# Kernel tuning notes

Measured on AMD Instinct MI355X. Metric: run time of the kernel, lower is better.

## Reference

```python
import jax, jax.numpy as jnp
import numpy as np

TAU = 0.05


def _normalize(x):
    return x / jnp.linalg.norm(x, axis=-1, keepdims=True)


def setup_inputs() -> dict:
    key = jax.random.key(0)
    ks = jax.random.split(key, 7)
    D, S, Q, N, P = 256, 64, 4096, 16384, 1024
    return {
        "article_emb": jax.random.normal(ks[0], (D,), dtype=jnp.float32),
        "section_embs": jax.random.normal(ks[1], (S, D), dtype=jnp.float32),
        "question_embs": jax.random.normal(ks[2], (Q, D), dtype=jnp.float32),
        "sentence_embs": jax.random.normal(ks[3], (N, D), dtype=jnp.float32),
        "paragraph_idx_for_question": jax.random.randint(ks[4], (Q,), 0, P, dtype=jnp.int32),
        "section_idx_for_question": jax.random.randint(ks[5], (Q,), 0, S, dtype=jnp.int32),
        "sent_paragraph_idx": jax.random.randint(ks[6], (N,), 0, P, dtype=jnp.int32),
        "num_paragraphs": P,
    }


def reference(article_emb, section_embs, question_embs, sentence_embs,
              paragraph_idx_for_question, section_idx_for_question,
              sent_paragraph_idx, num_paragraphs):
    tau = TAU
    dt = question_embs.dtype
    # normalize (article is normalized in the original but unused in the loss; AT_loss == 0)
    _ = _normalize(article_emb)
    sec = _normalize(section_embs)   # [S, D]
    que = _normalize(question_embs)  # [Q, D]
    sen = _normalize(sentence_embs)  # [N, D]
    Q, N = que.shape[0], sen.shape[0]
    S = sec.shape[0]

    # ---------- QS debiased InfoNCE ----------
    sim_qs = jnp.matmul(que, sen.T) / tau              # [Q, N]
    exp_qs = jnp.exp(sim_qs)                           # [Q, N]
    pos = paragraph_idx_for_question[:, None] == sent_paragraph_idx[None, :]  # [Q, N]
    M = pos.sum(axis=1)                                # positives per question
    Nn = N - M                                         # negatives per question
    sum_pos = jnp.where(pos, exp_qs, 0.0).sum(axis=1)
    sum_neg = exp_qs.sum(axis=1) - sum_pos
    eta_plus = 1.0 / max(int(num_paragraphs), 1)
    eta_minus = 1.0 - eta_plus
    min_val = jnp.exp(jnp.asarray(-1.0 / tau, dtype=dt))
    M_f = jnp.maximum(M, 1).astype(dt)
    Nn_f = jnp.maximum(Nn, 1).astype(dt)
    g = jnp.maximum((sum_neg / Nn_f - eta_plus * sum_pos / M_f) / eta_minus, min_val)  # [Q]
    valid = (M > 0) & (Nn > 0)                         # [Q]
    # -log(numer / (numer + N_neg * g)) = -(sim - log(denom))
    denom_qs = exp_qs + (Nn.astype(dt) * g)[:, None]
    log_ratio_qs = sim_qs - jnp.log(denom_qs)
    mask_qs = pos & valid[:, None]
    total_qs = jnp.where(valid, M, 0).sum()
    qs_loss = -jnp.where(mask_qs, log_ratio_qs, 0.0).sum()
    qs_loss = jnp.where(total_qs > 0, qs_loss / total_qs.astype(dt), jnp.asarray(0.0, dt))

    # ---------- SQ InfoNCE ----------
    sim_sq = jnp.matmul(sec, que.T) / tau              # [S, Q]
    exp_sq = jnp.exp(sim_sq)
    posq = section_idx_for_question[None, :] == jnp.arange(S)[:, None]  # [S, Q]
    Mq = posq.sum(axis=1)
    Nnq = Q - Mq
    sum_neg_q = exp_sq.sum(axis=1) - jnp.where(posq, exp_sq, 0.0).sum(axis=1)  # [S]
    log_ratio_sq = sim_sq - jnp.log(exp_sq + sum_neg_q[:, None])
    validq = (Mq > 0) & (Nnq > 0)
    mask_sq = posq & validq[:, None]
    total_sq = jnp.where(validq, Mq, 0).sum()
    sq_loss = -jnp.where(mask_sq, log_ratio_sq, 0.0).sum()
    sq_loss = jnp.where(total_sq > 0, sq_loss / total_sq.astype(dt), jnp.asarray(0.0, dt))

    return qs_loss + sq_loss
```

## Files before the change

### kernel.cpp

```cpp
#include <hip/hip_runtime.h>
#include <hip/hip_bf16.h>
#include <math.h>

#define D 256
#define INV_TAU 20.0f
#define CAP 64
#define PBUF 128
#define ACC2S (INV_TAU / 256.0f)
#define K2F (ACC2S * 1.4426950408889634f)

typedef __attribute__((ext_vector_type(4))) float f32x4;

#define GLOAD16(gp, lp) \
    __builtin_amdgcn_global_load_lds((const __attribute__((address_space(1))) void*)(gp), \
                                     (__attribute__((address_space(3))) void*)(lp), 16, 0, 0)

__global__ void norm_all(const float* __restrict__ que, const float* __restrict__ sen,
                         const float* __restrict__ sec,
                         unsigned char* __restrict__ queb, unsigned char* __restrict__ senb,
                         unsigned char* __restrict__ secb, int Q, int N, int S) {
    int r = blockIdx.x * 4 + (threadIdx.x >> 6);
    int lane = threadIdx.x & 63;
    if (r >= Q + N + S) return;
    const float* src; unsigned char* dst; int row;
    if (r < Q) { src = que; dst = queb; row = r; }
    else if (r < Q + N) { src = sen; dst = senb; row = r - Q; }
    else { src = sec; dst = secb; row = r - Q - N; }
    const float4* p = (const float4*)(src + (size_t)row * D);
    float4 v = p[lane];
    float ss = v.x * v.x + v.y * v.y + v.z * v.z + v.w * v.w;
    #pragma unroll
    for (int m = 1; m < 64; m <<= 1) ss += __shfl_xor(ss, m);
    float s = rsqrtf(ss) * 16.0f;
    int pk = __builtin_amdgcn_cvt_pk_fp8_f32(v.x * s, v.y * s, 0, false);
    pk = __builtin_amdgcn_cvt_pk_fp8_f32(v.z * s, v.w * s, pk, true);
    int wg = (lane >> 1) & 7;
    int pos = (wg < 4) ? (2 * wg) : (2 * (wg - 4) + 1);
    int byte = ((lane >> 4) << 6) + (pos << 3) + ((lane & 1) << 2);
    *(int*)(dst + (size_t)row * D + byte) = pk;
}

__global__ __launch_bounds__(256, 4)
void qs_sq(const unsigned char* __restrict__ queb, const unsigned char* __restrict__ senb,
           const unsigned char* __restrict__ secb,
           const int* __restrict__ pidq, const int* __restrict__ pidn,
           const int* __restrict__ sidx, int Q,
           float* __restrict__ partial, int* __restrict__ cnt, float* __restrict__ pos_s,
           float* __restrict__ sq_all, float* __restrict__ sq_pos, int* __restrict__ sq_m,
           float* __restrict__ simq) {
    __shared__ unsigned char As[128 * 64];
    __shared__ unsigned char Bs[128 * 64];
    __shared__ int pqs[128];
    __shared__ int pns[128];
    __shared__ float sums[2][128];
    __shared__ int lcnt;
    __shared__ int lq[PBUF];
    __shared__ float lsv[PBUF];

    const int tid = threadIdx.x;
    const int lane = tid & 63;
    const int cl = lane & 15;
    const int g = lane >> 4;
    const int wid = tid >> 6;
    const int bid = blockIdx.x;
    const int nsq = Q >> 7;

    if (bid < nsq) {
        const int q0 = bid * 128;
        const int qw = q0 + wid * 32;
        f32x4 acc[4][2];
        #pragma unroll
        for (int si = 0; si < 4; ++si)
            #pragma unroll
            for (int qi = 0; qi < 2; ++qi)
                acc[si][qi] = (f32x4){0.f, 0.f, 0.f, 0.f};
        const unsigned char* abase = secb + (size_t)cl * D + g * 16;
        const unsigned char* bbase = queb + (size_t)(qw + cl) * D + g * 16;
        #pragma unroll
        for (int b = 0; b < 4; ++b) {
            const int k0 = b * 64;
            long2 af[4], bq[2];
            #pragma unroll
            for (int si = 0; si < 4; ++si)
                af[si] = *(const long2*)(abase + (size_t)si * 16 * D + k0);
            #pragma unroll
            for (int qi = 0; qi < 2; ++qi)
                bq[qi] = *(const long2*)(bbase + (size_t)qi * 16 * D + k0);
            #pragma unroll
            for (int si = 0; si < 4; ++si)
                #pragma unroll
                for (int qi = 0; qi < 2; ++qi) {
                    acc[si][qi] = __builtin_amdgcn_mfma_f32_16x16x32_fp8_fp8(af[si].x, bq[qi].x, acc[si][qi], 0, 0, 0);
                    acc[si][qi] = __builtin_amdgcn_mfma_f32_16x16x32_fp8_fp8(af[si].y, bq[qi].y, acc[si][qi], 0, 0, 0);
                }
        }
        int sidxv[2];
        sidxv[0] = sidx[qw + cl];
        sidxv[1] = sidx[qw + 16 + cl];
        #pragma unroll
        for (int si = 0; si < 4; ++si) {
            float pa[4] = {0.f, 0.f, 0.f, 0.f};
            #pragma unroll
            for (int qi = 0; qi < 2; ++qi) {
                #pragma unroll
                for (int j = 0; j < 4; ++j) {
                    int srow = si * 16 + g * 4 + j;
                    float sv = acc[si][qi][j] * ACC2S;
                    float e = __expf(sv);
                    pa[j] += e;
                    if (sidxv[qi] == srow) {
                        int q = qw + qi * 16 + cl;
                        simq[q] = sv;
                        atomicAdd(&sq_pos[srow], e);
                        atomicAdd(&sq_m[srow], 1);
                    }
                }
            }
            #pragma unroll
            for (int j = 0; j < 4; ++j) {
                float a = pa[j];
                #pragma unroll
                for (int msk = 1; msk < 16; msk <<= 1) a += __shfl_xor(a, msk);
                if (cl == 0) atomicAdd(&sq_all[si * 16 + g * 4 + j], a);
            }
        }
        return;
    }

    const int qbid = bid - nsq;
    const int qt = qbid & 31;
    const int nt = qbid >> 5;
    const int wr = wid >> 1, wc = wid & 1;
    const int q0 = qt * 128;
    const int n0 = nt * 128;

    if (tid < 128) pqs[tid] = pidq[q0 + tid];
    else           pns[tid - 128] = pidn[n0 + tid - 128];
    if (tid == 0) lcnt = 0;

    const int r0s = tid >> 2;
    const int c0s = tid & 3;
    const unsigned char* qa0 = queb + (size_t)(q0 + r0s) * D + ((c0s ^ ((r0s >> 1) & 3)) << 4);
    const unsigned char* qa1 = queb + (size_t)(q0 + 64 + r0s) * D + ((c0s ^ (((r0s + 64) >> 1) & 3)) << 4);
    const unsigned char* sb0 = senb + (size_t)(n0 + r0s) * D + ((c0s ^ ((r0s >> 1) & 3)) << 4);
    const unsigned char* sb1 = senb + (size_t)(n0 + 64 + r0s) * D + ((c0s ^ (((r0s + 64) >> 1) & 3)) << 4);
    const int ld0 = wid * 1024;
    const int ld1 = 4096 + wid * 1024;

#define STAGE(k0) do { \
    GLOAD16(qa0 + (k0), &As[ld0]); \
    GLOAD16(qa1 + (k0), &As[ld1]); \
    GLOAD16(sb0 + (k0), &Bs[ld0]); \
    GLOAD16(sb1 + (k0), &Bs[ld1]); \
} while (0)

    f32x4 acc[4][4];
    #pragma unroll
    for (int m = 0; m < 4; ++m)
        #pragma unroll
        for (int n = 0; n < 4; ++n)
            acc[m][n] = (f32x4){0.f, 0.f, 0.f, 0.f};

    const int fsw = (g ^ ((cl >> 1) & 3)) << 4;
    int offA[4], offB[4];
    #pragma unroll
    for (int m = 0; m < 4; ++m) offA[m] = (wr * 64 + m * 16 + cl) * 64 + fsw;
    #pragma unroll
    for (int n = 0; n < 4; ++n) offB[n] = (wc * 64 + n * 16 + cl) * 64 + fsw;

    STAGE(0);
    #pragma unroll
    for (int ks = 0; ks < 4; ++ks) {
        __syncthreads();
        long2 af[4], bg[4];
        #pragma unroll
        for (int m = 0; m < 4; ++m) af[m] = *(const long2*)&As[offA[m]];
        #pragma unroll
        for (int n = 0; n < 4; ++n) bg[n] = *(const long2*)&Bs[offB[n]];
        #pragma unroll
        for (int m = 0; m < 4; ++m)
            #pragma unroll
            for (int n = 0; n < 4; ++n)
                acc[m][n] = __builtin_amdgcn_mfma_f32_16x16x32_fp8_fp8(af[m].x, bg[n].x, acc[m][n], 0, 0, 0);
        #pragma unroll
        for (int m = 0; m < 4; ++m)
            #pragma unroll
            for (int n = 0; n < 4; ++n)
                acc[m][n] = __builtin_amdgcn_mfma_f32_16x16x32_fp8_fp8(af[m].y, bg[n].y, acc[m][n], 0, 0, 0);
        if (ks < 3) {
            __syncthreads();
            STAGE((ks + 1) * 64);
        }
    }
#undef STAGE

    #pragma unroll
    for (int m = 0; m < 4; ++m) {
        float se[4] = {0.f, 0.f, 0.f, 0.f};
        int pqr[4];
        #pragma unroll
        for (int j = 0; j < 4; ++j) pqr[j] = pqs[wr * 64 + m * 16 + g * 4 + j];
        #pragma unroll
        for (int n = 0; n < 4; ++n) {
            const int pcol = pns[wc * 64 + n * 16 + cl];
            #pragma unroll
            for (int j = 0; j < 4; ++j) {
                float e = __builtin_amdgcn_exp2f(acc[m][n][j] * K2F);
                se[j] += e;
                if (pqr[j] == pcol) {
                    int li = atomicAdd(&lcnt, 1);
                    if (li < PBUF) {
                        lq[li] = q0 + wr * 64 + m * 16 + g * 4 + j;
                        lsv[li] = acc[m][n][j] * ACC2S;
                    }
                }
            }
        }
        #pragma unroll
        for (int j = 0; j < 4; ++j) {
            float a = se[j];
            #pragma unroll
            for (int msk = 1; msk < 16; msk <<= 1) a += __shfl_xor(a, msk);
            if (cl == 0) sums[wc][wr * 64 + m * 16 + g * 4 + j] = a;
        }
    }
    __syncthreads();
    if (tid < 128)
        partial[(size_t)nt * Q + q0 + tid] = sums[0][tid] + sums[1][tid];
    int nc = lcnt < PBUF ? lcnt : PBUF;
    for (int i = tid; i < nc; i += 256) {
        int q = lq[i];
        int idx = atomicAdd(&cnt[q], 1);
        if (idx < CAP) pos_s[(size_t)q * CAP + idx] = lsv[i];
    }
}

__global__ __launch_bounds__(256)
void finish(const float* __restrict__ partial, int NSLICE,
            const int* __restrict__ cnt, const float* __restrict__ pos_s,
            const int* __restrict__ sidx, const float* __restrict__ simq,
            const float* __restrict__ sq_all, const float* __restrict__ sq_pos,
            const int* __restrict__ sq_m,
            const int* __restrict__ npp, int Qn, int Ntot,
            float* __restrict__ bpart) {
    __shared__ float fred[4][4];
    const int tid = threadIdx.x, lane = tid & 63, wid = tid >> 6;
    const int q = blockIdx.x * 4 + wid;

    float Sa = 0.f;
    for (int nb = lane; nb < NSLICE; nb += 64) Sa += partial[(size_t)nb * Qn + q];
    #pragma unroll
    for (int m = 1; m < 64; m <<= 1) Sa += __shfl_xor(Sa, m);

    int M = cnt[q];
    int mc = M < CAP ? M : CAP;
    float s = 0.f, e = 0.f;
    if (lane < mc) { s = pos_s[(size_t)q * CAP + lane]; e = __expf(s); }
    float Sp = e;
    #pragma unroll
    for (int m = 1; m < 64; m <<= 1) Sp += __shfl_xor(Sp, m);

    int Nn = Ntot - M;
    int P = npp[0];
    float eta_p = 1.0f / (float)(P > 1 ? P : 1);
    float eta_m = 1.0f - eta_p;
    float Mf = (float)(M > 1 ? M : 1);
    float Nnf = (float)(Nn > 1 ? Nn : 1);
    float gg = fmaxf(((Sa - Sp) / Nnf - eta_p * Sp / Mf) / eta_m, __expf(-INV_TAU));
    float c = (float)Nn * gg;

    float contrib = (lane < mc) ? (s - __logf(e + c)) : 0.f;
    #pragma unroll
    for (int m = 1; m < 64; m <<= 1) contrib += __shfl_xor(contrib, m);

    if (lane == 0) {
        float qs_num = 0.f, qs_cnt = 0.f, sq_num = 0.f, sq_cnt = 0.f;
        if (M > 0 && Nn > 0) { qs_num = contrib; qs_cnt = (float)M; }
        int sct = sidx[q];
        int Mq = sq_m[sct];
        if (Mq > 0 && (Qn - Mq) > 0) {
            float sv = simq[q];
            float sumneg = sq_all[sct] - sq_pos[sct];
            sq_num = sv - __logf(__expf(sv) + sumneg);
            sq_cnt = 1.f;
        }
        fred[wid][0] = qs_num; fred[wid][1] = qs_cnt;
        fred[wid][2] = sq_num; fred[wid][3] = sq_cnt;
    }
    __syncthreads();
    if (tid < 4) {
        float v = fred[0][tid] + fred[1][tid] + fred[2][tid] + fred[3][tid];
        bpart[(size_t)blockIdx.x * 4 + tid] = v;
    }
}

__global__ void combine2(const float* __restrict__ bpart, int nblk, float* __restrict__ out) {
    __shared__ float r2[4][4];
    const int tid = threadIdx.x, lane = tid & 63, wid = tid >> 6;
    float v[4] = {0.f, 0.f, 0.f, 0.f};
    for (int i = tid; i < nblk; i += 256) {
        #pragma unroll
        for (int c2 = 0; c2 < 4; ++c2) v[c2] += bpart[(size_t)i * 4 + c2];
    }
    #pragma unroll
    for (int m = 1; m < 64; m <<= 1)
        #pragma unroll
        for (int c2 = 0; c2 < 4; ++c2) v[c2] += __shfl_xor(v[c2], m);
    if (lane == 0) {
        #pragma unroll
        for (int c2 = 0; c2 < 4; ++c2) r2[wid][c2] = v[c2];
    }
    __syncthreads();
    if (tid == 0) {
        float qs_num = r2[0][0] + r2[1][0] + r2[2][0] + r2[3][0];
        float qs_cnt = r2[0][1] + r2[1][1] + r2[2][1] + r2[3][1];
        float sq_num = r2[0][2] + r2[1][2] + r2[2][2] + r2[3][2];
        float sq_cnt = r2[0][3] + r2[1][3] + r2[2][3] + r2[3][3];
        float qs = qs_cnt > 0.f ? -qs_num / qs_cnt : 0.f;
        float sq = sq_cnt > 0.f ? -sq_num / sq_cnt : 0.f;
        out[0] = qs + sq;
    }
}

extern "C" void kernel_launch(void* const* d_in, const int* in_sizes, int n_in,
                              void* d_out, int out_size, void* d_ws, size_t ws_size,
                              hipStream_t stream) {
    const float* sec = (const float*)d_in[1];
    const float* que = (const float*)d_in[2];
    const float* sen = (const float*)d_in[3];
    const int* pidq = (const int*)d_in[4];
    const int* sidx = (const int*)d_in[5];
    const int* pidn = (const int*)d_in[6];
    const int* npp = (const int*)d_in[7];
    const int S = in_sizes[1] / D;
    const int Q = in_sizes[2] / D;
    const int N = in_sizes[3] / D;
    const int NB = N / 128;
    const int FBLK = Q / 4;

    char* p = (char*)d_ws;
    unsigned char* queb = (unsigned char*)p; p += (size_t)Q * D;
    unsigned char* senb = (unsigned char*)p; p += (size_t)N * D;
    unsigned char* secb = (unsigned char*)p; p += (size_t)S * D;
    p = (char*)(((uintptr_t)p + 255) & ~(uintptr_t)255);
    float* simq = (float*)p; p += (size_t)Q * 4;
    float* pos_s = (float*)p; p += (size_t)Q * CAP * 4;
    float* partial = (float*)p; p += (size_t)NB * Q * 4;
    float* bpart = (float*)p; p += (size_t)FBLK * 4 * 4;
    char* z0 = p;
    int* cnt = (int*)p; p += (size_t)Q * 4;
    float* sq_all = (float*)p; p += (size_t)S * 4;
    float* sq_pos = (float*)p; p += (size_t)S * 4;
    int* sq_m = (int*)p; p += (size_t)S * 4;
    size_t zbytes = (size_t)(p - z0);

    hipMemsetAsync(z0, 0, zbytes, stream);
    norm_all<<<(Q + N + S + 3) / 4, 256, 0, stream>>>(que, sen, sec, queb, senb, secb, Q, N, S);
    qs_sq<<<Q / 128 + (Q / 128) * NB, 256, 0, stream>>>(queb, senb, secb, pidq, pidn, sidx, Q,
                                                        partial, cnt, pos_s,
                                                        sq_all, sq_pos, sq_m, simq);
    finish<<<FBLK, 256, 0, stream>>>(partial, NB, cnt, pos_s, sidx, simq,
                                     sq_all, sq_pos, sq_m, npp, Q, N, bpart);
    combine2<<<1, 256, 0, stream>>>(bpart, FBLK, (float*)d_out);
}
```

Before: 86.28 us.

## Stage full K=256 tiles into LDS once instead of four K-chunk stages

Replaces the four-step K loop, which staged 64-byte K slices with a barrier pair around each, with a single bulk load of the full 128x256 fp8 tiles for A and B into LDS. A new XOR swizzle across sixteen 16-byte chunks matches the wider rows. This removes six barriers and the serialized load-then-compute steps per tile. In exchange LDS use grows to about 64KB per block, and launch bounds drop from 4 to 2 blocks per CU, reducing occupancy and the overlap of loads with compute across blocks.

```diff
diff --git a/kernel.cpp b/kernel.cpp
--- a/kernel.cpp
+++ b/kernel.cpp
@@ -40,7 +40,7 @@
     *(int*)(dst + (size_t)row * D + byte) = pk;
 }
 
-__global__ __launch_bounds__(256, 4)
+__global__ __launch_bounds__(256, 2)
 void qs_sq(const unsigned char* __restrict__ queb, const unsigned char* __restrict__ senb,
            const unsigned char* __restrict__ secb,
            const int* __restrict__ pidq, const int* __restrict__ pidn,
@@ -48,8 +48,8 @@
            float* __restrict__ partial, int* __restrict__ cnt, float* __restrict__ pos_s,
            float* __restrict__ sq_all, float* __restrict__ sq_pos, int* __restrict__ sq_m,
            float* __restrict__ simq) {
-    __shared__ unsigned char As[128 * 64];
-    __shared__ unsigned char Bs[128 * 64];
+    __shared__ unsigned char As[128 * 256];
+    __shared__ unsigned char Bs[128 * 256];
     __shared__ int pqs[128];
     __shared__ int pns[128];
     __shared__ float sums[2][128];
@@ -138,21 +138,18 @@
     else           pns[tid - 128] = pidn[n0 + tid - 128];
     if (tid == 0) lcnt = 0;
 
-    const int r0s = tid >> 2;
-    const int c0s = tid & 3;
-    const unsigned char* qa0 = queb + (size_t)(q0 + r0s) * D + ((c0s ^ ((r0s >> 1) & 3)) << 4);
-    const unsigned char* qa1 = queb + (size_t)(q0 + 64 + r0s) * D + ((c0s ^ (((r0s + 64) >> 1) & 3)) << 4);
-    const unsigned char* sb0 = senb + (size_t)(n0 + r0s) * D + ((c0s ^ ((r0s >> 1) & 3)) << 4);
-    const unsigned char* sb1 = senb + (size_t)(n0 + 64 + r0s) * D + ((c0s ^ (((r0s + 64) >> 1) & 3)) << 4);
-    const int ld0 = wid * 1024;
-    const int ld1 = 4096 + wid * 1024;
-
-#define STAGE(k0) do { \
-    GLOAD16(qa0 + (k0), &As[ld0]); \
-    GLOAD16(qa1 + (k0), &As[ld1]); \
-    GLOAD16(sb0 + (k0), &Bs[ld0]); \
-    GLOAD16(sb1 + (k0), &Bs[ld1]); \
-} while (0)
+    {
+        const int srow = tid >> 4;
+        const int swz = ((tid & 15) ^ (srow & 7)) << 4;
+        const unsigned char* qa = queb + (size_t)(q0 + srow) * D + swz;
+        const unsigned char* sb = senb + (size_t)(n0 + srow) * D + swz;
+        #pragma unroll
+        for (int j = 0; j < 8; ++j) {
+            GLOAD16(qa + (size_t)j * 16 * D, &As[j * 4096 + wid * 1024]);
+            GLOAD16(sb + (size_t)j * 16 * D, &Bs[j * 4096 + wid * 1024]);
+        }
+    }
+    __syncthreads();
 
     f32x4 acc[4][4];
     #pragma unroll
@@ -161,22 +158,21 @@
         for (int n = 0; n < 4; ++n)
             acc[m][n] = (f32x4){0.f, 0.f, 0.f, 0.f};
 
-    const int fsw = (g ^ ((cl >> 1) & 3)) << 4;
-    int offA[4], offB[4];
-    #pragma unroll
-    for (int m = 0; m < 4; ++m) offA[m] = (wr * 64 + m * 16 + cl) * 64 + fsw;
-    #pragma unroll
-    for (int n = 0; n < 4; ++n) offB[n] = (wc * 64 + n * 16 + cl) * 64 + fsw;
-
-    STAGE(0);
-    #pragma unroll
-    for (int ks = 0; ks < 4; ++ks) {
-        __syncthreads();
+    const int fx = cl & 7;
+    int rA[4], rB[4];
+    #pragma unroll
+    for (int m = 0; m < 4; ++m) rA[m] = (wr * 64 + m * 16 + cl) * 256;
+    #pragma unroll
+    for (int n = 0; n < 4; ++n) rB[n] = (wc * 64 + n * 16 + cl) * 256;
+
+    #pragma unroll
+    for (int blk = 0; blk < 4; ++blk) {
+        const int co = ((blk * 4 + g) ^ fx) << 4;
         long2 af[4], bg[4];
         #pragma unroll
-        for (int m = 0; m < 4; ++m) af[m] = *(const long2*)&As[offA[m]];
-        #pragma unroll
-        for (int n = 0; n < 4; ++n) bg[n] = *(const long2*)&Bs[offB[n]];
+        for (int m = 0; m < 4; ++m) af[m] = *(const long2*)&As[rA[m] + co];
+        #pragma unroll
+        for (int n = 0; n < 4; ++n) bg[n] = *(const long2*)&Bs[rB[n] + co];
         #pragma unroll
         for (int m = 0; m < 4; ++m)
             #pragma unroll
@@ -187,12 +183,7 @@
             #pragma unroll
             for (int n = 0; n < 4; ++n)
                 acc[m][n] = __builtin_amdgcn_mfma_f32_16x16x32_fp8_fp8(af[m].y, bg[n].y, acc[m][n], 0, 0, 0);
-        if (ks < 3) {
-            __syncthreads();
-            STAGE((ks + 1) * 64);
-        }
-    }
-#undef STAGE
+    }
 
     #pragma unroll
     for (int m = 0; m < 4; ++m) {
```

Measured after the change: 115.3 us. 33.7% more time.
